# Optimization experiments

Measured on AMD Instinct MI355X. Metric: run time of the kernel, lower is better.

## Reference

```python
import jax, jax.numpy as jnp
import numpy as np

N_NODES = 100000
N_EDGES = 600000
IN_DIM = 128
HID = 128
N_GRAPHS = 512
N_CLASSES = 10


def setup_inputs() -> dict:
    key = jax.random.key(0)
    ks = jax.random.split(key, 8)
    feats = jax.random.normal(ks[0], (N_NODES, IN_DIM), dtype=jnp.float32)
    W = jax.random.normal(ks[1], (IN_DIM, HID), dtype=jnp.float32) * 0.05
    b = jnp.zeros((HID,), dtype=jnp.float32)
    W1 = jax.random.normal(ks[2], (HID, 12), dtype=jnp.float32) * 0.05
    b1 = jnp.zeros((12,), dtype=jnp.float32)
    W2 = jax.random.normal(ks[3], (12, N_CLASSES), dtype=jnp.float32) * 0.05
    b2 = jnp.zeros((N_CLASSES,), dtype=jnp.float32)
    src = jax.random.randint(ks[4], (N_EDGES,), 0, N_NODES, dtype=jnp.int32)
    dst = jax.random.randint(ks[5], (N_EDGES,), 0, N_NODES, dtype=jnp.int32)
    graph_ids = jnp.sort(jax.random.randint(ks[6], (N_NODES,), 0, N_GRAPHS, dtype=jnp.int32))
    return {"feats": feats, "W": W, "b": b, "W1": W1, "b1": b1, "W2": W2,
            "b2": b2, "src": src, "dst": dst, "graph_ids": graph_ids}


def reference(feats, W, b, W1, b1, W2, b2, src, dst, graph_ids):
    ones_e = jnp.ones((src.shape[0],), dtype=feats.dtype)
    # DGL GraphConv norm='both': clamp degrees to >= 1
    out_deg = jnp.maximum(jax.ops.segment_sum(ones_e, src, num_segments=N_NODES), 1.0)
    in_deg = jnp.maximum(jax.ops.segment_sum(ones_e, dst, num_segments=N_NODES), 1.0)
    norm_src = out_deg ** -0.5  # [N]
    norm_dst = in_deg ** -0.5
    x = feats * norm_src[:, None]               # scale source features
    agg = jax.ops.segment_sum(x[src], dst, num_segments=N_NODES)  # gather-scatter SpMM
    h = agg * norm_dst[:, None]
    h = jnp.maximum(h @ W + b, 0.0)             # GraphConv linear + ReLU  [N, HID]
    # mean_nodes: per-graph segment mean (empty graphs -> 0, matching DGL)
    gsum = jax.ops.segment_sum(h, graph_ids, num_segments=N_GRAPHS)
    cnt = jax.ops.segment_sum(jnp.ones((N_NODES,), h.dtype), graph_ids, num_segments=N_GRAPHS)
    hg = jnp.where(cnt[:, None] > 0, gsum / jnp.maximum(cnt, 1.0)[:, None], 0.0)
    # tiny 2-layer MLP classifier
    return (hg @ W1 + b1) @ W2 + b2             # [N_GRAPHS, N_CLASSES]
```

## Files before the change

kernel.cpp:

```cpp
#include <hip/hip_runtime.h>
#include <hip/hip_fp16.h>

#define N_NODES 100000
#define N_EDGES 600000
#define DIM 128
#define N_GRAPHS 512
#define MLP_HID 12
#define N_CLASSES 10
#define NPB 16
#define SLOT_CAP 32
#define TPAD 136

#define WFRAG_BLOCKS 8
#define CONV_BLOCKS 6250
#define EDGE2_ITEMS (N_EDGES / 2)
#define EDGE2_BLOCKS ((EDGE2_ITEMS + 255) / 256)

typedef _Float16 half8 __attribute__((ext_vector_type(8)));
typedef float float4v __attribute__((ext_vector_type(4)));
typedef float floatx2 __attribute__((ext_vector_type(2)));

__global__ void prep_kernel(const float* __restrict__ W, __half* __restrict__ wfrag,
                            const float4* __restrict__ feats4, int2* __restrict__ feats_q,
                            const int* __restrict__ src, const int* __restrict__ dst,
                            int* __restrict__ out_hist, int* __restrict__ in_hist,
                            int* __restrict__ slots) {
    int bx = blockIdx.x;
    if (bx < WFRAG_BLOCKS) {
        int item = bx * 256 + threadIdx.x;
        if (item < 2048) {
            int lane = item & 63;
            int kt = (item >> 6) & 3;
            int nt = item >> 8;
            int n = nt * 16 + (lane & 15);
            int k0 = kt * 32 + (lane >> 4) * 8;
            union { int4 i4; __half h[8]; } u;
            #pragma unroll
            for (int j = 0; j < 8; ++j) u.h[j] = __float2half(W[(k0 + j) * DIM + n]);
            ((int4*)wfrag)[item] = u.i4;
        }
        return;
    }
    bx -= WFRAG_BLOCKS;
    if (bx < CONV_BLOCKS) {
        int i = bx * 256 + threadIdx.x;
        float4 a = feats4[2 * i];
        float4 c = feats4[2 * i + 1];
        int lo = __builtin_amdgcn_cvt_pk_fp8_f32(a.x, a.y, 0, false);
        lo     = __builtin_amdgcn_cvt_pk_fp8_f32(a.z, a.w, lo, true);
        int hi = __builtin_amdgcn_cvt_pk_fp8_f32(c.x, c.y, 0, false);
        hi     = __builtin_amdgcn_cvt_pk_fp8_f32(c.z, c.w, hi, true);
        feats_q[i] = make_int2(lo, hi);
        return;
    }
    bx -= CONV_BLOCKS;
    int i = bx * 256 + threadIdx.x;
    if (i < EDGE2_ITEMS) {
        int2 s2 = ((const int2*)src)[i];
        int2 d2 = ((const int2*)dst)[i];
        atomicAdd(&out_hist[s2.x], 1);
        atomicAdd(&out_hist[s2.y], 1);
        int t0 = atomicAdd(&in_hist[d2.x], 1);
        int t1 = atomicAdd(&in_hist[d2.y], 1);
        if (t0 < SLOT_CAP) __builtin_nontemporal_store(s2.x, &slots[d2.x * SLOT_CAP + t0]);
        if (t1 < SLOT_CAP) __builtin_nontemporal_store(s2.y, &slots[d2.y * SLOT_CAP + t1]);
    }
}

__global__ __launch_bounds__(128) void fused_gemm(
        const int* __restrict__ feats_q,
        const int* __restrict__ in_hist, const int* __restrict__ out_hist,
        const int* __restrict__ slots, const __half* __restrict__ wfrag,
        const float* __restrict__ bvec, const int* __restrict__ gid,
        float* __restrict__ gsum, float* __restrict__ cnt) {
    __shared__ __half tile_h[NPB][TPAD];
    int t = threadIdx.x;
    int group = t >> 5;
    int lane = t & 31;
    int node0 = blockIdx.x * NPB;

    int dv = 0;
    if (lane < 16) dv = in_hist[node0 + lane];
    int deg[4]; int es[4];
    #pragma unroll
    for (int r = 0; r < 4; ++r) {
        int j = r * 4 + group;
        deg[r] = __shfl(dv, j, 32);
        es[r] = 0;
        if (lane < min(deg[r], SLOT_CAP)) es[r] = slots[(node0 + j) * SLOT_CAP + lane];
    }
    float ns[4];
    #pragma unroll
    for (int r = 0; r < 4; ++r) {
        ns[r] = 0.0f;
        if (lane < min(deg[r], SLOT_CAP)) ns[r] = rsqrtf((float)max(out_hist[es[r]], 1));
    }

    #pragma unroll
    for (int r = 0; r < 4; ++r) {
        int j = r * 4 + group;
        int m = min(deg[r], SLOT_CAP);
        float4 a4 = make_float4(0.f, 0.f, 0.f, 0.f);
        int i = 0;
        for (; i + 4 <= m; i += 4) {
            int sn0 = __shfl(es[r], i + 0, 32), sn1 = __shfl(es[r], i + 1, 32);
            int sn2 = __shfl(es[r], i + 2, 32), sn3 = __shfl(es[r], i + 3, 32);
            float n0 = __shfl(ns[r], i + 0, 32), n1 = __shfl(ns[r], i + 1, 32);
            float n2 = __shfl(ns[r], i + 2, 32), n3 = __shfl(ns[r], i + 3, 32);
            int q0 = feats_q[sn0 * 32 + lane];
            int q1 = feats_q[sn1 * 32 + lane];
            int q2 = feats_q[sn2 * 32 + lane];
            int q3 = feats_q[sn3 * 32 + lane];
            floatx2 p0 = __builtin_amdgcn_cvt_pk_f32_fp8(q0, false);
            floatx2 r0 = __builtin_amdgcn_cvt_pk_f32_fp8(q0, true);
            floatx2 p1 = __builtin_amdgcn_cvt_pk_f32_fp8(q1, false);
            floatx2 r1 = __builtin_amdgcn_cvt_pk_f32_fp8(q1, true);
            floatx2 p2 = __builtin_amdgcn_cvt_pk_f32_fp8(q2, false);
            floatx2 r2 = __builtin_amdgcn_cvt_pk_f32_fp8(q2, true);
            floatx2 p3 = __builtin_amdgcn_cvt_pk_f32_fp8(q3, false);
            floatx2 r3 = __builtin_amdgcn_cvt_pk_f32_fp8(q3, true);
            a4.x = fmaf(p0[0], n0, a4.x); a4.y = fmaf(p0[1], n0, a4.y);
            a4.z = fmaf(r0[0], n0, a4.z); a4.w = fmaf(r0[1], n0, a4.w);
            a4.x = fmaf(p1[0], n1, a4.x); a4.y = fmaf(p1[1], n1, a4.y);
            a4.z = fmaf(r1[0], n1, a4.z); a4.w = fmaf(r1[1], n1, a4.w);
            a4.x = fmaf(p2[0], n2, a4.x); a4.y = fmaf(p2[1], n2, a4.y);
            a4.z = fmaf(r2[0], n2, a4.z); a4.w = fmaf(r2[1], n2, a4.w);
            a4.x = fmaf(p3[0], n3, a4.x); a4.y = fmaf(p3[1], n3, a4.y);
            a4.z = fmaf(r3[0], n3, a4.z); a4.w = fmaf(r3[1], n3, a4.w);
        }
        for (; i < m; ++i) {
            int sn = __shfl(es[r], i, 32);
            float nv = __shfl(ns[r], i, 32);
            int q = feats_q[sn * 32 + lane];
            floatx2 p = __builtin_amdgcn_cvt_pk_f32_fp8(q, false);
            floatx2 rr = __builtin_amdgcn_cvt_pk_f32_fp8(q, true);
            a4.x = fmaf(p[0], nv, a4.x); a4.y = fmaf(p[1], nv, a4.y);
            a4.z = fmaf(rr[0], nv, a4.z); a4.w = fmaf(rr[1], nv, a4.w);
        }
        float nd = rsqrtf((float)max(deg[r], 1));
        union { int2 v; __half2 h2[2]; } st;
        st.h2[0] = __floats2half2_rn(a4.x * nd, a4.y * nd);
        st.h2[1] = __floats2half2_rn(a4.z * nd, a4.w * nd);
        *(int2*)&tile_h[j][lane * 4] = st.v;
    }
    __syncthreads();

    int wave = t >> 6;
    int wl = t & 63;
    int quad = wl >> 4;
    int col = wl & 15;

    half8 afrag[4];
    #pragma unroll
    for (int kt = 0; kt < 4; ++kt)
        afrag[kt] = *reinterpret_cast<const half8*>(&tile_h[col][kt * 32 + quad * 8]);

    float4v c[4];
    #pragma unroll
    for (int nt = 0; nt < 4; ++nt) { c[nt][0] = 0.f; c[nt][1] = 0.f; c[nt][2] = 0.f; c[nt][3] = 0.f; }

    #pragma unroll
    for (int nt = 0; nt < 4; ++nt) {
        int ntile = wave * 4 + nt;
        #pragma unroll
        for (int kt = 0; kt < 4; ++kt) {
            half8 bfrag = *reinterpret_cast<const half8*>(wfrag + ((size_t)(ntile * 4 + kt) * 64 + wl) * 8);
            c[nt] = __builtin_amdgcn_mfma_f32_16x16x32_f16(afrag[kt], bfrag, c[nt], 0, 0, 0);
        }
    }

    int g0 = gid[node0];
    if (gid[node0 + NPB - 1] == g0) {
        #pragma unroll
        for (int nt = 0; nt < 4; ++nt) {
            float bb = bvec[(wave * 4 + nt) * 16 + col];
            float v = 0.f;
            #pragma unroll
            for (int i2 = 0; i2 < 4; ++i2) v += fmaxf(c[nt][i2] + bb, 0.f);
            v += __shfl_xor(v, 16, 64);
            v += __shfl_xor(v, 32, 64);
            if (wl < 16) atomicAdd(&gsum[g0 * DIM + (wave * 4 + nt) * 16 + col], v);
        }
        if (t == 0) atomicAdd(&cnt[g0], (float)NPB);
    } else {
        #pragma unroll
        for (int nt = 0; nt < 4; ++nt) {
            float bb = bvec[(wave * 4 + nt) * 16 + col];
            #pragma unroll
            for (int i2 = 0; i2 < 4; ++i2) {
                int g = gid[node0 + quad * 4 + i2];
                atomicAdd(&gsum[g * DIM + (wave * 4 + nt) * 16 + col],
                          fmaxf(c[nt][i2] + bb, 0.f));
            }
        }
        if (wave == 0 && col == 0) {
            #pragma unroll
            for (int i2 = 0; i2 < 4; ++i2)
                atomicAdd(&cnt[gid[node0 + quad * 4 + i2]], 1.0f);
        }
    }
}

__global__ __launch_bounds__(128) void mlp_kernel(
        const float* __restrict__ gsum, const float* __restrict__ cnt,
        const float* __restrict__ W1, const float* __restrict__ b1,
        const float* __restrict__ W2, const float* __restrict__ b2,
        float* __restrict__ out) {
    __shared__ float s[DIM];
    __shared__ float t1[MLP_HID];
    int g = blockIdx.x;
    int t = threadIdx.x;
    float c = cnt[g];
    s[t] = (c > 0.0f) ? (gsum[g * DIM + t] / c) : 0.0f;
    __syncthreads();
    if (t < MLP_HID) {
        float a = b1[t];
        for (int k = 0; k < DIM; ++k) a = fmaf(s[k], W1[k * MLP_HID + t], a);
        t1[t] = a;
    }
    __syncthreads();
    if (t < N_CLASSES) {
        float o = b2[t];
        #pragma unroll
        for (int j = 0; j < MLP_HID; ++j) o = fmaf(t1[j], W2[j * N_CLASSES + t], o);
        out[g * N_CLASSES + t] = o;
    }
}

extern "C" void kernel_launch(void* const* d_in, const int* in_sizes, int n_in,
                              void* d_out, int out_size, void* d_ws, size_t ws_size,
                              hipStream_t stream) {
    const float* feats = (const float*)d_in[0];
    const float* W     = (const float*)d_in[1];
    const float* b     = (const float*)d_in[2];
    const float* W1    = (const float*)d_in[3];
    const float* b1    = (const float*)d_in[4];
    const float* W2    = (const float*)d_in[5];
    const float* b2    = (const float*)d_in[6];
    const int*   src   = (const int*)d_in[7];
    const int*   dst   = (const int*)d_in[8];
    const int*   gid   = (const int*)d_in[9];
    float* out = (float*)d_out;

    char* ws = (char*)d_ws;
    int*   out_hist = (int*)ws;   ws += (size_t)N_NODES * 4;
    int*   in_hist  = (int*)ws;   ws += (size_t)N_NODES * 4;
    float* gsum     = (float*)ws; ws += (size_t)N_GRAPHS * DIM * 4;
    float* cnt      = (float*)ws; ws += (size_t)N_GRAPHS * 4;
    size_t zero_bytes = (size_t)(ws - (char*)d_ws);
    ws = (char*)(((uintptr_t)ws + 255) & ~(uintptr_t)255);
    int*    slots   = (int*)ws;    ws += (size_t)N_NODES * SLOT_CAP * 4;
    int*    feats_q = (int*)ws;    ws += (size_t)N_NODES * DIM;
    __half* wfrag   = (__half*)ws; ws += (size_t)2048 * 8 * 2;

    hipMemsetAsync(d_ws, 0, zero_bytes, stream);

    prep_kernel<<<WFRAG_BLOCKS + CONV_BLOCKS + EDGE2_BLOCKS, 256, 0, stream>>>(
        W, wfrag, (const float4*)feats, (int2*)feats_q,
        src, dst, out_hist, in_hist, slots);

    fused_gemm<<<N_NODES / NPB, 128, 0, stream>>>(
        feats_q, in_hist, out_hist, slots, wfrag, b, gid, gsum, cnt);

    mlp_kernel<<<N_GRAPHS, 128, 0, stream>>>(gsum, cnt, W1, b1, W2, b2, out);
}
```

Baseline: 217.5 us.

## Merge prep, aggregation-GEMM and MLP into one persistent kernel with grid barriers

Replaces the three kernel launches with a single persistent kernel of 1024 blocks that uses grid-stride loops for quantisation and edge histogramming. Atomic-counter grid barriers separate those phases from the aggregation/MFMA phase and from the MLP. Each 256-thread block now handles two 16-node tiles at once. This is meant to remove launch gaps and tail effects between kernels. In exchange it relies on all 1024 blocks being co-resident, otherwise the barrier spin-wait deadlocks, and it adds barrier latency and reduces the parallelism of the prep phase.

Result: slower. 593.2 us (+172.7%).

```diff
diff --git a/kernel.cpp b/kernel.cpp
--- a/kernel.cpp
+++ b/kernel.cpp
@@ -7,57 +7,67 @@
 #define N_GRAPHS 512
 #define MLP_HID 12
 #define N_CLASSES 10
-#define NPB 16
 #define SLOT_CAP 32
 #define TPAD 136
 
-#define WFRAG_BLOCKS 8
-#define CONV_BLOCKS 6250
+#define NBLK 1024
+#define NTHR 256
+#define GTHREADS (NBLK * NTHR)
+#define CONV_ITEMS (N_NODES * DIM / 8)
 #define EDGE2_ITEMS (N_EDGES / 2)
-#define EDGE2_BLOCKS ((EDGE2_ITEMS + 255) / 256)
+#define NTILE2 (N_NODES / 32)
 
 typedef _Float16 half8 __attribute__((ext_vector_type(8)));
 typedef float float4v __attribute__((ext_vector_type(4)));
 typedef float floatx2 __attribute__((ext_vector_type(2)));
 
-__global__ void prep_kernel(const float* __restrict__ W, __half* __restrict__ wfrag,
-                            const float4* __restrict__ feats4, int2* __restrict__ feats_q,
-                            const int* __restrict__ src, const int* __restrict__ dst,
-                            int* __restrict__ out_hist, int* __restrict__ in_hist,
-                            int* __restrict__ slots) {
-    int bx = blockIdx.x;
-    if (bx < WFRAG_BLOCKS) {
-        int item = bx * 256 + threadIdx.x;
-        if (item < 2048) {
-            int lane = item & 63;
-            int kt = (item >> 6) & 3;
-            int nt = item >> 8;
-            int n = nt * 16 + (lane & 15);
-            int k0 = kt * 32 + (lane >> 4) * 8;
-            union { int4 i4; __half h[8]; } u;
-            #pragma unroll
-            for (int j = 0; j < 8; ++j) u.h[j] = __float2half(W[(k0 + j) * DIM + n]);
-            ((int4*)wfrag)[item] = u.i4;
-        }
-        return;
-    }
-    bx -= WFRAG_BLOCKS;
-    if (bx < CONV_BLOCKS) {
-        int i = bx * 256 + threadIdx.x;
-        float4 a = feats4[2 * i];
-        float4 c = feats4[2 * i + 1];
+__device__ __forceinline__ void grid_barrier(int* __restrict__ bar, int target) {
+    __syncthreads();
+    if (threadIdx.x == 0) {
+        __hip_atomic_fetch_add(bar, 1, __ATOMIC_ACQ_REL, __HIP_MEMORY_SCOPE_AGENT);
+        while (__hip_atomic_load(bar, __ATOMIC_ACQUIRE, __HIP_MEMORY_SCOPE_AGENT) < target)
+            __builtin_amdgcn_s_sleep(8);
+    }
+    __syncthreads();
+}
+
+__global__ __launch_bounds__(NTHR, 4) void mega_kernel(
+        const float* __restrict__ W, __half* __restrict__ wfrag,
+        const float4v* __restrict__ feats4, int2* __restrict__ feats_q,
+        const int2* __restrict__ src2, const int2* __restrict__ dst2,
+        int* __restrict__ out_hist, int* __restrict__ in_hist,
+        int* __restrict__ slots,
+        const float* __restrict__ bvec, const int* __restrict__ gid,
+        float* __restrict__ gsum, float* __restrict__ cnt,
+        const float* __restrict__ W1, const float* __restrict__ b1,
+        const float* __restrict__ W2, const float* __restrict__ b2,
+        float* __restrict__ out, int* __restrict__ bar) {
+    const int tid = threadIdx.x;
+    const int gtid = blockIdx.x * NTHR + tid;
+
+    if (gtid < 2048) {
+        int lane = gtid & 63;
+        int kt = (gtid >> 6) & 3;
+        int nt = gtid >> 8;
+        int n = nt * 16 + (lane & 15);
+        int k0 = kt * 32 + (lane >> 4) * 8;
+        union { int4 i4; __half h[8]; } u;
+        #pragma unroll
+        for (int j = 0; j < 8; ++j) u.h[j] = __float2half(W[(k0 + j) * DIM + n]);
+        ((int4*)wfrag)[gtid] = u.i4;
+    }
+    for (int i = gtid; i < CONV_ITEMS; i += GTHREADS) {
+        float4v a = feats4[2 * i];
+        float4v c = feats4[2 * i + 1];
         int lo = __builtin_amdgcn_cvt_pk_fp8_f32(a.x, a.y, 0, false);
         lo     = __builtin_amdgcn_cvt_pk_fp8_f32(a.z, a.w, lo, true);
         int hi = __builtin_amdgcn_cvt_pk_fp8_f32(c.x, c.y, 0, false);
         hi     = __builtin_amdgcn_cvt_pk_fp8_f32(c.z, c.w, hi, true);
         feats_q[i] = make_int2(lo, hi);
-        return;
-    }
-    bx -= CONV_BLOCKS;
-    int i = bx * 256 + threadIdx.x;
-    if (i < EDGE2_ITEMS) {
-        int2 s2 = ((const int2*)src)[i];
-        int2 d2 = ((const int2*)dst)[i];
+    }
+    for (int i = gtid; i < EDGE2_ITEMS; i += GTHREADS) {
+        int2 s2 = src2[i];
+        int2 d2 = dst2[i];
         atomicAdd(&out_hist[s2.x], 1);
         atomicAdd(&out_hist[s2.y], 1);
         int t0 = atomicAdd(&in_hist[d2.x], 1);
@@ -65,165 +75,161 @@
         if (t0 < SLOT_CAP) __builtin_nontemporal_store(s2.x, &slots[d2.x * SLOT_CAP + t0]);
         if (t1 < SLOT_CAP) __builtin_nontemporal_store(s2.y, &slots[d2.y * SLOT_CAP + t1]);
     }
-}
-
-__global__ __launch_bounds__(128) void fused_gemm(
-        const int* __restrict__ feats_q,
-        const int* __restrict__ in_hist, const int* __restrict__ out_hist,
-        const int* __restrict__ slots, const __half* __restrict__ wfrag,
-        const float* __restrict__ bvec, const int* __restrict__ gid,
-        float* __restrict__ gsum, float* __restrict__ cnt) {
-    __shared__ __half tile_h[NPB][TPAD];
-    int t = threadIdx.x;
-    int group = t >> 5;
-    int lane = t & 31;
-    int node0 = blockIdx.x * NPB;
-
-    int dv = 0;
-    if (lane < 16) dv = in_hist[node0 + lane];
-    int deg[4]; int es[4];
-    #pragma unroll
-    for (int r = 0; r < 4; ++r) {
-        int j = r * 4 + group;
-        deg[r] = __shfl(dv, j, 32);
-        es[r] = 0;
-        if (lane < min(deg[r], SLOT_CAP)) es[r] = slots[(node0 + j) * SLOT_CAP + lane];
-    }
-    float ns[4];
-    #pragma unroll
-    for (int r = 0; r < 4; ++r) {
-        ns[r] = 0.0f;
-        if (lane < min(deg[r], SLOT_CAP)) ns[r] = rsqrtf((float)max(out_hist[es[r]], 1));
-    }
-
-    #pragma unroll
-    for (int r = 0; r < 4; ++r) {
-        int j = r * 4 + group;
-        int m = min(deg[r], SLOT_CAP);
-        float4 a4 = make_float4(0.f, 0.f, 0.f, 0.f);
-        int i = 0;
-        for (; i + 4 <= m; i += 4) {
-            int sn0 = __shfl(es[r], i + 0, 32), sn1 = __shfl(es[r], i + 1, 32);
-            int sn2 = __shfl(es[r], i + 2, 32), sn3 = __shfl(es[r], i + 3, 32);
-            float n0 = __shfl(ns[r], i + 0, 32), n1 = __shfl(ns[r], i + 1, 32);
-            float n2 = __shfl(ns[r], i + 2, 32), n3 = __shfl(ns[r], i + 3, 32);
-            int q0 = feats_q[sn0 * 32 + lane];
-            int q1 = feats_q[sn1 * 32 + lane];
-            int q2 = feats_q[sn2 * 32 + lane];
-            int q3 = feats_q[sn3 * 32 + lane];
-            floatx2 p0 = __builtin_amdgcn_cvt_pk_f32_fp8(q0, false);
-            floatx2 r0 = __builtin_amdgcn_cvt_pk_f32_fp8(q0, true);
-            floatx2 p1 = __builtin_amdgcn_cvt_pk_f32_fp8(q1, false);
-            floatx2 r1 = __builtin_amdgcn_cvt_pk_f32_fp8(q1, true);
-            floatx2 p2 = __builtin_amdgcn_cvt_pk_f32_fp8(q2, false);
-            floatx2 r2 = __builtin_amdgcn_cvt_pk_f32_fp8(q2, true);
-            floatx2 p3 = __builtin_amdgcn_cvt_pk_f32_fp8(q3, false);
-            floatx2 r3 = __builtin_amdgcn_cvt_pk_f32_fp8(q3, true);
-            a4.x = fmaf(p0[0], n0, a4.x); a4.y = fmaf(p0[1], n0, a4.y);
-            a4.z = fmaf(r0[0], n0, a4.z); a4.w = fmaf(r0[1], n0, a4.w);
-            a4.x = fmaf(p1[0], n1, a4.x); a4.y = fmaf(p1[1], n1, a4.y);
-            a4.z = fmaf(r1[0], n1, a4.z); a4.w = fmaf(r1[1], n1, a4.w);
-            a4.x = fmaf(p2[0], n2, a4.x); a4.y = fmaf(p2[1], n2, a4.y);
-            a4.z = fmaf(r2[0], n2, a4.z); a4.w = fmaf(r2[1], n2, a4.w);
-            a4.x = fmaf(p3[0], n3, a4.x); a4.y = fmaf(p3[1], n3, a4.y);
-            a4.z = fmaf(r3[0], n3, a4.z); a4.w = fmaf(r3[1], n3, a4.w);
-        }
-        for (; i < m; ++i) {
-            int sn = __shfl(es[r], i, 32);
-            float nv = __shfl(ns[r], i, 32);
-            int q = feats_q[sn * 32 + lane];
-            floatx2 p = __builtin_amdgcn_cvt_pk_f32_fp8(q, false);
-            floatx2 rr = __builtin_amdgcn_cvt_pk_f32_fp8(q, true);
-            a4.x = fmaf(p[0], nv, a4.x); a4.y = fmaf(p[1], nv, a4.y);
-            a4.z = fmaf(rr[0], nv, a4.z); a4.w = fmaf(rr[1], nv, a4.w);
-        }
-        float nd = rsqrtf((float)max(deg[r], 1));
-        union { int2 v; __half2 h2[2]; } st;
-        st.h2[0] = __floats2half2_rn(a4.x * nd, a4.y * nd);
-        st.h2[1] = __floats2half2_rn(a4.z * nd, a4.w * nd);
-        *(int2*)&tile_h[j][lane * 4] = st.v;
-    }
-    __syncthreads();
-
-    int wave = t >> 6;
-    int wl = t & 63;
-    int quad = wl >> 4;
-    int col = wl & 15;
-
-    half8 afrag[4];
-    #pragma unroll
-    for (int kt = 0; kt < 4; ++kt)
-        afrag[kt] = *reinterpret_cast<const half8*>(&tile_h[col][kt * 32 + quad * 8]);
-
-    float4v c[4];
-    #pragma unroll
-    for (int nt = 0; nt < 4; ++nt) { c[nt][0] = 0.f; c[nt][1] = 0.f; c[nt][2] = 0.f; c[nt][3] = 0.f; }
-
-    #pragma unroll
-    for (int nt = 0; nt < 4; ++nt) {
-        int ntile = wave * 4 + nt;
-        #pragma unroll
-        for (int kt = 0; kt < 4; ++kt) {
-            half8 bfrag = *reinterpret_cast<const half8*>(wfrag + ((size_t)(ntile * 4 + kt) * 64 + wl) * 8);
-            c[nt] = __builtin_amdgcn_mfma_f32_16x16x32_f16(afrag[kt], bfrag, c[nt], 0, 0, 0);
-        }
-    }
-
-    int g0 = gid[node0];
-    if (gid[node0 + NPB - 1] == g0) {
+
+    grid_barrier(bar, NBLK);
+
+    __shared__ __half tile_h[2][16][TPAD];
+    const int half_id = tid >> 7;
+    const int th = tid & 127;
+    const int group = th >> 5;
+    const int lane = th & 31;
+    const int wave = th >> 6;
+    const int wl = th & 63;
+    const int quad = wl >> 4;
+    const int col = wl & 15;
+
+    for (int tp = blockIdx.x; tp < NTILE2; tp += NBLK) {
+        int node0 = tp * 32 + half_id * 16;
+
+        int dv = 0;
+        if (lane < 16) dv = in_hist[node0 + lane];
+        int deg[4]; int es[4];
+        #pragma unroll
+        for (int r = 0; r < 4; ++r) {
+            int j = r * 4 + group;
+            deg[r] = __shfl(dv, j, 32);
+            es[r] = 0;
+            if (lane < min(deg[r], SLOT_CAP)) es[r] = slots[(node0 + j) * SLOT_CAP + lane];
+        }
+        float ns[4];
+        #pragma unroll
+        for (int r = 0; r < 4; ++r) {
+            ns[r] = 0.0f;
+            if (lane < min(deg[r], SLOT_CAP)) ns[r] = rsqrtf((float)max(out_hist[es[r]], 1));
+        }
+
+        #pragma unroll
+        for (int r = 0; r < 4; ++r) {
+            int j = r * 4 + group;
+            int m = min(deg[r], SLOT_CAP);
+            float4 a4 = make_float4(0.f, 0.f, 0.f, 0.f);
+            int i = 0;
+            for (; i + 4 <= m; i += 4) {
+                int sn0 = __shfl(es[r], i + 0, 32), sn1 = __shfl(es[r], i + 1, 32);
+                int sn2 = __shfl(es[r], i + 2, 32), sn3 = __shfl(es[r], i + 3, 32);
+                float n0 = __shfl(ns[r], i + 0, 32), n1 = __shfl(ns[r], i + 1, 32);
+                float n2 = __shfl(ns[r], i + 2, 32), n3 = __shfl(ns[r], i + 3, 32);
+                int q0 = ((const int*)feats_q)[sn0 * 32 + lane];
+                int q1 = ((const int*)feats_q)[sn1 * 32 + lane];
+                int q2 = ((const int*)feats_q)[sn2 * 32 + lane];
+                int q3 = ((const int*)feats_q)[sn3 * 32 + lane];
+                floatx2 p0 = __builtin_amdgcn_cvt_pk_f32_fp8(q0, false);
+                floatx2 r0 = __builtin_amdgcn_cvt_pk_f32_fp8(q0, true);
+                floatx2 p1 = __builtin_amdgcn_cvt_pk_f32_fp8(q1, false);
+                floatx2 r1 = __builtin_amdgcn_cvt_pk_f32_fp8(q1, true);
+                floatx2 p2 = __builtin_amdgcn_cvt_pk_f32_fp8(q2, false);
+                floatx2 r2 = __builtin_amdgcn_cvt_pk_f32_fp8(q2, true);
+                floatx2 p3 = __builtin_amdgcn_cvt_pk_f32_fp8(q3, false);
+                floatx2 r3 = __builtin_amdgcn_cvt_pk_f32_fp8(q3, true);
+                a4.x = fmaf(p0[0], n0, a4.x); a4.y = fmaf(p0[1], n0, a4.y);
+                a4.z = fmaf(r0[0], n0, a4.z); a4.w = fmaf(r0[1], n0, a4.w);
+                a4.x = fmaf(p1[0], n1, a4.x); a4.y = fmaf(p1[1], n1, a4.y);
+                a4.z = fmaf(r1[0], n1, a4.z); a4.w = fmaf(r1[1], n1, a4.w);
+                a4.x = fmaf(p2[0], n2, a4.x); a4.y = fmaf(p2[1], n2, a4.y);
+                a4.z = fmaf(r2[0], n2, a4.z); a4.w = fmaf(r2[1], n2, a4.w);
+                a4.x = fmaf(p3[0], n3, a4.x); a4.y = fmaf(p3[1], n3, a4.y);
+                a4.z = fmaf(r3[0], n3, a4.z); a4.w = fmaf(r3[1], n3, a4.w);
+            }
+            for (; i < m; ++i) {
+                int sn = __shfl(es[r], i, 32);
+                float nv = __shfl(ns[r], i, 32);
+                int q = ((const int*)feats_q)[sn * 32 + lane];
+                floatx2 p = __builtin_amdgcn_cvt_pk_f32_fp8(q, false);
+                floatx2 rr = __builtin_amdgcn_cvt_pk_f32_fp8(q, true);
+                a4.x = fmaf(p[0], nv, a4.x); a4.y = fmaf(p[1], nv, a4.y);
+                a4.z = fmaf(rr[0], nv, a4.z); a4.w = fmaf(rr[1], nv, a4.w);
+            }
+            float nd = rsqrtf((float)max(deg[r], 1));
+            union { int2 v; __half2 h2[2]; } st;
+            st.h2[0] = __floats2half2_rn(a4.x * nd, a4.y * nd);
+            st.h2[1] = __floats2half2_rn(a4.z * nd, a4.w * nd);
+            *(int2*)&tile_h[half_id][j][lane * 4] = st.v;
+        }
+        __syncthreads();
+
+        half8 afrag[4];
+        #pragma unroll
+        for (int kt = 0; kt < 4; ++kt)
+            afrag[kt] = *reinterpret_cast<const half8*>(&tile_h[half_id][col][kt * 32 + quad * 8]);
+
+        float4v c[4];
+        #pragma unroll
+        for (int nt = 0; nt < 4; ++nt) { c[nt][0] = 0.f; c[nt][1] = 0.f; c[nt][2] = 0.f; c[nt][3] = 0.f; }
+
         #pragma unroll
         for (int nt = 0; nt < 4; ++nt) {
-            float bb = bvec[(wave * 4 + nt) * 16 + col];
-            float v = 0.f;
-            #pragma unroll
-            for (int i2 = 0; i2 < 4; ++i2) v += fmaxf(c[nt][i2] + bb, 0.f);
-            v += __shfl_xor(v, 16, 64);
-            v += __shfl_xor(v, 32, 64);
-            if (wl < 16) atomicAdd(&gsum[g0 * DIM + (wave * 4 + nt) * 16 + col], v);
-        }
-        if (t == 0) atomicAdd(&cnt[g0], (float)NPB);
-    } else {
-        #pragma unroll
-        for (int nt = 0; nt < 4; ++nt) {
-            float bb = bvec[(wave * 4 + nt) * 16 + col];
-            #pragma unroll
-            for (int i2 = 0; i2 < 4; ++i2) {
-                int g = gid[node0 + quad * 4 + i2];
-                atomicAdd(&gsum[g * DIM + (wave * 4 + nt) * 16 + col],
-                          fmaxf(c[nt][i2] + bb, 0.f));
-            }
-        }
-        if (wave == 0 && col == 0) {
-            #pragma unroll
-            for (int i2 = 0; i2 < 4; ++i2)
-                atomicAdd(&cnt[gid[node0 + quad * 4 + i2]], 1.0f);
-        }
-    }
-}
-
-__global__ __launch_bounds__(128) void mlp_kernel(
-        const float* __restrict__ gsum, const float* __restrict__ cnt,
-        const float* __restrict__ W1, const float* __restrict__ b1,
-        const float* __restrict__ W2, const float* __restrict__ b2,
-        float* __restrict__ out) {
-    __shared__ float s[DIM];
-    __shared__ float t1[MLP_HID];
-    int g = blockIdx.x;
-    int t = threadIdx.x;
-    float c = cnt[g];
-    s[t] = (c > 0.0f) ? (gsum[g * DIM + t] / c) : 0.0f;
-    __syncthreads();
-    if (t < MLP_HID) {
-        float a = b1[t];
-        for (int k = 0; k < DIM; ++k) a = fmaf(s[k], W1[k * MLP_HID + t], a);
-        t1[t] = a;
-    }
-    __syncthreads();
-    if (t < N_CLASSES) {
-        float o = b2[t];
-        #pragma unroll
-        for (int j = 0; j < MLP_HID; ++j) o = fmaf(t1[j], W2[j * N_CLASSES + t], o);
-        out[g * N_CLASSES + t] = o;
+            int ntile = wave * 4 + nt;
+            #pragma unroll
+            for (int kt = 0; kt < 4; ++kt) {
+                half8 bfrag = *reinterpret_cast<const half8*>(wfrag + ((size_t)(ntile * 4 + kt) * 64 + wl) * 8);
+                c[nt] = __builtin_amdgcn_mfma_f32_16x16x32_f16(afrag[kt], bfrag, c[nt], 0, 0, 0);
+            }
+        }
+
+        int g0 = gid[node0];
+        if (gid[node0 + 15] == g0) {
+            #pragma unroll
+            for (int nt = 0; nt < 4; ++nt) {
+                float bb = bvec[(wave * 4 + nt) * 16 + col];
+                float v = 0.f;
+                #pragma unroll
+                for (int i2 = 0; i2 < 4; ++i2) v += fmaxf(c[nt][i2] + bb, 0.f);
+                v += __shfl_xor(v, 16, 64);
+                v += __shfl_xor(v, 32, 64);
+                if (wl < 16) atomicAdd(&gsum[g0 * DIM + (wave * 4 + nt) * 16 + col], v);
+            }
+            if (th == 0) atomicAdd(&cnt[g0], 16.0f);
+        } else {
+            #pragma unroll
+            for (int nt = 0; nt < 4; ++nt) {
+                float bb = bvec[(wave * 4 + nt) * 16 + col];
+                #pragma unroll
+                for (int i2 = 0; i2 < 4; ++i2) {
+                    int g = gid[node0 + quad * 4 + i2];
+                    atomicAdd(&gsum[g * DIM + (wave * 4 + nt) * 16 + col],
+                              fmaxf(c[nt][i2] + bb, 0.f));
+                }
+            }
+            if (wave == 0 && col == 0) {
+                #pragma unroll
+                for (int i2 = 0; i2 < 4; ++i2)
+                    atomicAdd(&cnt[gid[node0 + quad * 4 + i2]], 1.0f);
+            }
+        }
+        __syncthreads();
+    }
+
+    grid_barrier(bar, 2 * NBLK);
+
+    if (blockIdx.x < N_GRAPHS) {
+        __shared__ float s[DIM];
+        __shared__ float t1[MLP_HID];
+        int g = blockIdx.x;
+        float cv = cnt[g];
+        if (tid < DIM) s[tid] = (cv > 0.0f) ? (gsum[g * DIM + tid] / cv) : 0.0f;
+        __syncthreads();
+        if (tid < MLP_HID) {
+            float a = b1[tid];
+            for (int k = 0; k < DIM; ++k) a = fmaf(s[k], W1[k * MLP_HID + tid], a);
+            t1[tid] = a;
+        }
+        __syncthreads();
+        if (tid < N_CLASSES) {
+            float o = b2[tid];
+            #pragma unroll
+            for (int j = 0; j < MLP_HID; ++j) o = fmaf(t1[j], W2[j * N_CLASSES + tid], o);
+            out[g * N_CLASSES + tid] = o;
+        }
     }
 }
 
@@ -247,6 +253,7 @@
     int*   in_hist  = (int*)ws;   ws += (size_t)N_NODES * 4;
     float* gsum     = (float*)ws; ws += (size_t)N_GRAPHS * DIM * 4;
     float* cnt      = (float*)ws; ws += (size_t)N_GRAPHS * 4;
+    int*   bar      = (int*)ws;   ws += 256;
     size_t zero_bytes = (size_t)(ws - (char*)d_ws);
     ws = (char*)(((uintptr_t)ws + 255) & ~(uintptr_t)255);
     int*    slots   = (int*)ws;    ws += (size_t)N_NODES * SLOT_CAP * 4;
@@ -255,12 +262,8 @@
 
     hipMemsetAsync(d_ws, 0, zero_bytes, stream);
 
-    prep_kernel<<<WFRAG_BLOCKS + CONV_BLOCKS + EDGE2_BLOCKS, 256, 0, stream>>>(
-        W, wfrag, (const float4*)feats, (int2*)feats_q,
-        src, dst, out_hist, in_hist, slots);
-
-    fused_gemm<<<N_NODES / NPB, 128, 0, stream>>>(
-        feats_q, in_hist, out_hist, slots, wfrag, b, gid, gsum, cnt);
-
-    mlp_kernel<<<N_GRAPHS, 128, 0, stream>>>(gsum, cnt, W1, b1, W2, b2, out);
+    mega_kernel<<<NBLK, NTHR, 0, stream>>>(
+        W, wfrag, (const float4v*)feats, (int2*)feats_q,
+        (const int2*)src, (const int2*)dst, out_hist, in_hist, slots,
+        b, gid, gsum, cnt, W1, b1, W2, b2, out, bar);
 }
```
